# Kernel tuning notes

Hardware: AMD Instinct MI355X
Metric: run time of the kernel (lower is better)

## Reference

```python
import jax, jax.numpy as jnp
import numpy as np

K = 10      # neighbors; conv width math 10 -> 3 -> 1
EPS = 1e-5  # InstanceNorm2d default eps (affine=False)
NEG = 0.2   # leaky relu slope


def _instnorm(x):
    m = x.mean(axis=(2, 3), keepdims=True)
    v = x.var(axis=(2, 3), keepdims=True)  # biased var, as in torch instance_norm
    return (x - m) * jax.lax.rsqrt(v + EPS)


def _conv13(x, w, b, s):
    y = jax.lax.conv_general_dilated(x, w, (1, s), 'VALID',
                                     dimension_numbers=('NCHW', 'OIHW', 'NCHW'))
    return y + b[None, :, None, None]


def _block(x, wA, bA, wB, bB):
    # Sequential(conv(1,3,stride(1,3)), IN, ReLU, conv(1,3), IN, ReLU)
    y = jax.nn.relu(_instnorm(_conv13(x, wA, bA, 3)))
    return jax.nn.relu(_instnorm(_conv13(y, wB, bB, 1)))


def _knn_idx(coords, k):
    # coords [B,2,N] -> k nearest neighbor indices [B,N,k] (self excluded)
    pts = coords.transpose(0, 2, 1)
    sq = (pts ** 2).sum(-1)
    dist = sq[:, :, None] + sq[:, None, :] - 2.0 * jnp.einsum('bnc,bmc->bnm', pts, pts)
    dist = jnp.clip(dist, 1e-12)
    _, idx = jax.lax.top_k(-dist, k + 1)  # smallest distances, sorted
    return idx[:, :, 1:]


def _gather_nb(x, idx):
    # x [B,C,N], idx [B,N,k] -> [B,C,N,k]
    return jax.vmap(lambda f, i: f[:, i])(x, idx)


def _graph_feat(feats, idx):
    nb = _gather_nb(feats, idx)
    ctr = jnp.broadcast_to(feats[..., None], nb.shape)
    return jnp.concatenate([ctr, nb - ctr], axis=1)  # [B,2C,N,k]


def _cos_angle(coords, idx):
    nei = _gather_nb(coords, idx)          # [B,2,N,k]
    ctr = coords[..., None]                # [B,2,N,1]
    dot = (ctr * nei).sum(axis=1, keepdims=True)
    na = jnp.sqrt((ctr ** 2).sum(axis=1, keepdims=True))
    nb = jnp.sqrt((nei ** 2).sum(axis=1, keepdims=True))
    return dot / (na * nb)                 # [B,1,N,k]


def _c1(w, x):
    # 1x1 conv, no bias
    return jnp.einsum('oi,bihw->bohw', w, x)


def _forward(coords, features, W1, W2, W3, W3o, a1wA, a1bA, a1wB, a1bB,
             a2wA, a2bA, a2wB, a2bB, angwA, angbA, angwB, angbB):
    B, C, N = features.shape
    lrelu = lambda x: jax.nn.leaky_relu(x, NEG)
    x0 = features[..., None]
    # KNN depends only on coords: all three torch graph builds give identical indices
    idx = _knn_idx(coords, K)
    x1_old = _graph_feat(features, idx)                         # [B,2C,N,K]
    x1 = _block(x1_old, a1wA, a1bA, a1wB, a1bB)                 # [B,C,N,1]
    # angle_enc1 is shared and idx identical -> f_ang1 == f_ang2
    f_ang = _block(_cos_angle(coords, idx), angwA, angbA, angwB, angbB)
    x2 = _block(_graph_feat(x1[..., 0], idx), a2wA, a2bA, a2wB, a2bB)
    x3 = jnp.concatenate([x0, x1 + f_ang, x2 + f_ang], axis=1)  # [B,3C,N,1]
    x3 = lrelu(_instnorm(_c1(W3, x3))).reshape(B, -1, N)
    x1o = lrelu(_instnorm(_c1(W1, x1_old))).max(axis=-1, keepdims=True)   # [B,C,N,1]
    x2o = lrelu(_instnorm(_c1(W2, _graph_feat(x1o[..., 0], idx)))).max(axis=-1, keepdims=True)
    x3o = jnp.concatenate([x0, x1o, x2o], axis=1)               # [B,4C,N,1]
    x3o = lrelu(_instnorm(_c1(W3o, x3o))).reshape(B, -1, N)
    return x3 + x3o


def setup_inputs():
    key = jax.random.key(0)
    ks = jax.random.split(key, 20)
    B, C, N = 4, 128, 4096
    r = lambda i, shp, sc=1.0: jax.random.normal(ks[i], shp, jnp.float32) * sc
    s = 0.05
    return {
        'coords': r(0, (B, 2, N)),
        'features': r(1, (B, C, N)),
        'W1': r(2, (C, 2 * C), s),
        'W2': r(3, (2 * C, 2 * C), s),
        'W3': r(4, (C, 3 * C), s),
        'W3o': r(5, (C, 4 * C), s),
        'a1wA': r(6, (C, 2 * C, 1, 3), s), 'a1bA': r(7, (C,), s),
        'a1wB': r(8, (C, C, 1, 3), s), 'a1bB': r(9, (C,), s),
        'a2wA': r(10, (C, 2 * C, 1, 3), s), 'a2bA': r(11, (C,), s),
        'a2wB': r(12, (C, C, 1, 3), s), 'a2bB': r(13, (C,), s),
        'angwA': r(14, (C, 1, 1, 3), s), 'angbA': r(15, (C,), s),
        'angwB': r(16, (C, C, 1, 3), s), 'angbB': r(17, (C,), s),
    }


def reference(coords, features, W1, W2, W3, W3o, a1wA, a1bA, a1wB, a1bB,
              a2wA, a2bA, a2wB, a2bB, angwA, angbA, angwB, angbB):
    return _forward(coords, features, W1, W2, W3, W3o, a1wA, a1bA, a1wB, a1bB,
                    a2wA, a2bA, a2wB, a2bB, angwA, angbA, angwB, angbB)
```

## Files before the change

kernel.cpp:

```cpp
#include <hip/hip_runtime.h>
#include <hip/hip_bf16.h>

typedef unsigned long long ull;

#define BN 4
#define CH 128
#define NP 4096
#define KNB 10
#define EPSI 1e-5f
#define GM_PTS 16
#define CA_PTS 16

#define FMA4(A, W, F) do { (A).x += (W).x*(F); (A).y += (W).y*(F); \
                           (A).z += (W).z*(F); (A).w += (W).w*(F); } while(0)

__device__ __forceinline__ ull shfl_xor_u64(ull v, int mask) {
    unsigned lo = (unsigned)(v & 0xFFFFFFFFu);
    unsigned hi = (unsigned)(v >> 32);
    lo = __shfl_xor(lo, mask);
    hi = __shfl_xor(hi, mask);
    return ((ull)hi << 32) | lo;
}

__device__ __forceinline__ int clampj(int j) { return ((unsigned)j < (unsigned)NP) ? j : 0; }

__device__ __forceinline__ unsigned short f2bf(float f) {
    unsigned u = __float_as_uint(f);
    unsigned r = u + 0x7FFFu + ((u >> 16) & 1u);
    return (unsigned short)(r >> 16);
}
__device__ __forceinline__ float bf2f(unsigned short h) {
    return __uint_as_float(((unsigned)h) << 16);
}
__device__ __forceinline__ float4 bfload4(const unsigned short* p) {
    ushort4 h = *(const ushort4*)p;
    float4 r; r.x = bf2f(h.x); r.y = bf2f(h.y); r.z = bf2f(h.z); r.w = bf2f(h.w);
    return r;
}

__device__ __forceinline__ void d_packA(const float* w, unsigned short* WT, int i) {
    int co = i % CH, ci = (i / CH) % CH, s = i / (CH * CH);
    float val;
    if (s == 0) {
        val = 0.f;
        for (int dk = 0; dk < 3; dk++)
            val += w[(co * 256 + ci) * 3 + dk] - w[(co * 256 + 128 + ci) * 3 + dk];
    } else {
        val = w[(co * 256 + 128 + ci) * 3 + (s - 1)];
    }
    WT[i] = f2bf(val);
}
__device__ __forceinline__ void d_packB(const float* w, float* WT, int i) {
    int co = i % CH, ci = (i / CH) % CH, dk = i / (CH * CH);
    WT[i] = w[(co * CH + ci) * 3 + dk];
}
__device__ __forceinline__ void d_packUV(const float* w, float* Wu, float* Wn, int Cout, int i) {
    int co = i % Cout, ci = i / Cout;
    float a = w[co * 256 + ci], bb = w[co * 256 + 128 + ci];
    Wu[i] = a - bb; Wn[i] = bb;
}
__device__ __forceinline__ void d_packP(const float* w, float* WT, int Cin, int Cout, int i) {
    int co = i % Cout, ci = i / Cout;
    WT[i] = w[co * Cin + ci];
}

__global__ void pack_all(const float* __restrict__ a1wA, const float* __restrict__ a2wA,
                         const float* __restrict__ a1wB, const float* __restrict__ a2wB,
                         const float* __restrict__ angwB, const float* __restrict__ W1,
                         const float* __restrict__ W2, const float* __restrict__ W3,
                         const float* __restrict__ W3o, const float* __restrict__ angwA,
                         float* __restrict__ WA1T, float* __restrict__ WA2T,
                         float* __restrict__ WB1T, float* __restrict__ WB2T,
                         float* __restrict__ WBAT,
                         float* __restrict__ W1U, float* __restrict__ W1N,
                         float* __restrict__ W2U, float* __restrict__ W2N,
                         float* __restrict__ W3T, float* __restrict__ W3OT,
                         float* __restrict__ WANGA) {
    int i = blockIdx.x * 256 + threadIdx.x;
    const int sA = 4 * CH * CH;
    const int sB = 3 * CH * CH;
    if (i < sA) { d_packA(a1wA, (unsigned short*)WA1T, i); return; } i -= sA;
    if (i < sA) { d_packA(a2wA, (unsigned short*)WA2T, i); return; } i -= sA;
    if (i < sB) { d_packB(a1wB, WB1T, i); return; } i -= sB;
    if (i < sB) { d_packB(a2wB, WB2T, i); return; } i -= sB;
    if (i < sB) { d_packB(angwB, WBAT, i); return; } i -= sB;
    if (i < CH * CH) { d_packUV(W1, W1U, W1N, CH, i); return; } i -= CH * CH;
    if (i < CH * 256) { d_packUV(W2, W2U, W2N, 256, i); return; } i -= CH * 256;
    if (i < 384 * CH) { d_packP(W3, W3T, 384, CH, i); return; } i -= 384 * CH;
    if (i < 512 * CH) { d_packP(W3o, W3OT, 512, CH, i); return; } i -= 512 * CH;
    if (i < 3 * CH) { d_packP(angwA, WANGA, 3, CH, i); return; }
}

__global__ void ftrans_kernel(const float* __restrict__ feats, float* __restrict__ F) {
    int i = blockIdx.x * 256 + threadIdx.x;
    if (i >= BN * CH * NP) return;
    int n = i % NP, c = (i / NP) % CH, b = i / (NP * CH);
    F[(b * NP + n) * CH + c] = feats[i];
}

__global__ void knn_kernel(const float* __restrict__ coords, int* __restrict__ IDX) {
    int gw = blockIdx.x * 4 + (threadIdx.x >> 6);
    int b = gw / NP;
    int n = gw % NP;
    int lane = threadIdx.x & 63;
    float xn = coords[(b * 2 + 0) * NP + n];
    float yn = coords[(b * 2 + 1) * NP + n];
    float sn = __fadd_rn(__fmul_rn(xn, xn), __fmul_rn(yn, yn));
    ull a[11];
    #pragma unroll
    for (int q = 0; q < 11; q++) a[q] = 0xFFFFFFFFFFFFFFFFULL;
    for (int m = lane; m < NP; m += 64) {
        float xm = coords[(b * 2 + 0) * NP + m];
        float ym = coords[(b * 2 + 1) * NP + m];
        float sm = __fadd_rn(__fmul_rn(xm, xm), __fmul_rn(ym, ym));
        float dot = __fmaf_rn(yn, ym, __fmul_rn(xn, xm));
        float d = __fsub_rn(__fadd_rn(sn, sm), __fmul_rn(2.0f, dot));
        d = fmaxf(d, 1e-12f);
        ull key = ((ull)__float_as_uint(d) << 32) | (unsigned)m;
        if (key < a[10]) {
            a[10] = key;
            #pragma unroll
            for (int q = 10; q > 0; --q)
                if (a[q] < a[q - 1]) { ull t = a[q]; a[q] = a[q - 1]; a[q - 1] = t; }
        }
    }
    for (int r = 0; r < 11; ++r) {
        ull k = a[0];
        ull mk = k;
        #pragma unroll
        for (int off = 1; off < 64; off <<= 1) {
            ull o = shfl_xor_u64(mk, off);
            mk = (o < mk) ? o : mk;
        }
        if (k == mk) {
            #pragma unroll
            for (int q = 0; q < 10; ++q) a[q] = a[q + 1];
            a[10] = 0xFFFFFFFFFFFFFFFFULL;
        }
        if (lane == 0 && r > 0) IDX[(b * NP + n) * KNB + (r - 1)] = (int)(mk & 0xFFFFFFFFu);
    }
}

__global__ void cosangle_kernel(const float* __restrict__ coords, const int* __restrict__ IDX,
                                float* __restrict__ COSA) {
    int i = blockIdx.x * 256 + threadIdx.x;
    if (i >= BN * NP * KNB) return;
    int n = (i / KNB) % NP, b = i / (KNB * NP);
    int j = clampj(IDX[i]);
    float xc = coords[(b * 2 + 0) * NP + n], yc = coords[(b * 2 + 1) * NP + n];
    float xm = coords[(b * 2 + 0) * NP + j], ym = coords[(b * 2 + 1) * NP + j];
    float dot = xc * xm + yc * ym;
    float na = sqrtf(xc * xc + yc * yc);
    float nb2 = sqrtf(xm * xm + ym * ym);
    COSA[i] = dot / fmaxf(na * nb2, 1e-30f);
}

__global__ __launch_bounds__(256) void convA_kernel(const float* __restrict__ Fin,
                             const int* __restrict__ IDX,
                             const float* __restrict__ WT, float* __restrict__ YA,
                             float* __restrict__ PART,
                             const float* __restrict__ STATS, int slot) {
    __shared__ __align__(16) float ctr[CA_PTS][CH];
    __shared__ __align__(16) unsigned short nbh[CA_PTS][9][CH];
    __shared__ int jidx[CA_PTS * 9];
    int b = blockIdx.x / (NP / CA_PTS);
    int chunk = blockIdx.x % (NP / CA_PTS);
    int n0 = chunk * CA_PTS;
    int cog = threadIdx.x & 31;
    int pg  = threadIdx.x >> 5;
    const float* SB = (slot >= 0) ? &STATS[((size_t)(slot * BN + b) * 256) * 2] : nullptr;
    if (threadIdx.x < CA_PTS * 9) {
        int n = threadIdx.x / 9, kk = threadIdx.x % 9;
        jidx[threadIdx.x] = clampj(IDX[(b * NP + n0 + n) * KNB + kk]);
    }
    __syncthreads();
    for (int v4 = threadIdx.x; v4 < CA_PTS * 32; v4 += 256) {
        int n = v4 >> 5, c4 = v4 & 31;
        float4 x = *(const float4*)&Fin[(size_t)(b * NP + n0 + n) * CH + c4 * 4];
        if (SB) {
            float4 s0 = *(const float4*)&SB[c4 * 8];
            float4 s1 = *(const float4*)&SB[c4 * 8 + 4];
            x.x = fmaxf((x.x - s0.x) * s0.y, 0.f);
            x.y = fmaxf((x.y - s0.z) * s0.w, 0.f);
            x.z = fmaxf((x.z - s1.x) * s1.y, 0.f);
            x.w = fmaxf((x.w - s1.z) * s1.w, 0.f);
        }
        *(float4*)&ctr[n][c4 * 4] = x;
    }
    for (int v4 = threadIdx.x; v4 < CA_PTS * 9 * 32; v4 += 256) {
        int n = v4 / 288, rem = v4 % 288, kk = rem >> 5, c4 = rem & 31;
        float4 x = *(const float4*)&Fin[(size_t)(b * NP + jidx[n * 9 + kk]) * CH + c4 * 4];
        if (SB) {
            float4 s0 = *(const float4*)&SB[c4 * 8];
            float4 s1 = *(const float4*)&SB[c4 * 8 + 4];
            x.x = fmaxf((x.x - s0.x) * s0.y, 0.f);
            x.y = fmaxf((x.y - s0.z) * s0.w, 0.f);
            x.z = fmaxf((x.z - s1.x) * s1.y, 0.f);
            x.w = fmaxf((x.w - s1.z) * s1.w, 0.f);
        }
        ushort4 h;
        h.x = f2bf(x.x); h.y = f2bf(x.y); h.z = f2bf(x.z); h.w = f2bf(x.w);
        *(ushort4*)&nbh[n][kk][c4 * 4] = h;
    }
    __syncthreads();
    const ushort4* W4 = (const ushort4*)WT;
    const int p0 = pg * 2, p1 = pg * 2 + 1;
    float4 cacc0, cacc1;
    cacc0.x = cacc0.y = cacc0.z = cacc0.w = 0.f;
    cacc1 = cacc0;
    for (int ci = 0; ci < CH; ci += 4) {
        float4 xa = *(const float4*)&ctr[p0][ci];
        float4 xb = *(const float4*)&ctr[p1][ci];
        #pragma unroll
        for (int u = 0; u < 4; ++u) {
            ushort4 hw = W4[(ci + u) * 32 + cog];
            float4 w; w.x = bf2f(hw.x); w.y = bf2f(hw.y); w.z = bf2f(hw.z); w.w = bf2f(hw.w);
            float fa = ((const float*)&xa)[u];
            float fb = ((const float*)&xb)[u];
            FMA4(cacc0, w, fa); FMA4(cacc1, w, fb);
        }
    }
    float4 t00 = cacc0, t01 = cacc0, t02 = cacc0;
    float4 t10 = cacc1, t11 = cacc1, t12 = cacc1;
    for (int dk = 0; dk < 3; ++dk) {
        const ushort4* Wd = W4 + (size_t)(1 + dk) * (CH * 32);
        const unsigned short* a00 = &nbh[p0][0 * 3 + dk][0];
        const unsigned short* a01 = &nbh[p0][1 * 3 + dk][0];
        const unsigned short* a02 = &nbh[p0][2 * 3 + dk][0];
        const unsigned short* a10 = &nbh[p1][0 * 3 + dk][0];
        const unsigned short* a11 = &nbh[p1][1 * 3 + dk][0];
        const unsigned short* a12 = &nbh[p1][2 * 3 + dk][0];
        for (int ci = 0; ci < CH; ci += 4) {
            float4 x00 = bfload4(&a00[ci]);
            float4 x01 = bfload4(&a01[ci]);
            float4 x02 = bfload4(&a02[ci]);
            float4 x10 = bfload4(&a10[ci]);
            float4 x11 = bfload4(&a11[ci]);
            float4 x12 = bfload4(&a12[ci]);
            #pragma unroll
            for (int u = 0; u < 4; ++u) {
                ushort4 hw = Wd[(ci + u) * 32 + cog];
                float4 w; w.x = bf2f(hw.x); w.y = bf2f(hw.y); w.z = bf2f(hw.z); w.w = bf2f(hw.w);
                FMA4(t00, w, ((const float*)&x00)[u]);
                FMA4(t01, w, ((const float*)&x01)[u]);
                FMA4(t02, w, ((const float*)&x02)[u]);
                FMA4(t10, w, ((const float*)&x10)[u]);
                FMA4(t11, w, ((const float*)&x11)[u]);
                FMA4(t12, w, ((const float*)&x12)[u]);
            }
        }
    }
    {
        size_t base0 = ((size_t)(b * NP + n0 + p0) * 3) * CH + cog * 4;
        *(float4*)&YA[base0 + 0 * CH] = t00;
        *(float4*)&YA[base0 + 1 * CH] = t01;
        *(float4*)&YA[base0 + 2 * CH] = t02;
        size_t base1 = ((size_t)(b * NP + n0 + p1) * 3) * CH + cog * 4;
        *(float4*)&YA[base1 + 0 * CH] = t10;
        *(float4*)&YA[base1 + 1 * CH] = t11;
        *(float4*)&YA[base1 + 2 * CH] = t12;
    }
    float s4[4], q4[4];
    s4[0] = t00.x + t01.x + t02.x + t10.x + t11.x + t12.x;
    s4[1] = t00.y + t01.y + t02.y + t10.y + t11.y + t12.y;
    s4[2] = t00.z + t01.z + t02.z + t10.z + t11.z + t12.z;
    s4[3] = t00.w + t01.w + t02.w + t10.w + t11.w + t12.w;
    q4[0] = t00.x*t00.x + t01.x*t01.x + t02.x*t02.x + t10.x*t10.x + t11.x*t11.x + t12.x*t12.x;
    q4[1] = t00.y*t00.y + t01.y*t01.y + t02.y*t02.y + t10.y*t10.y + t11.y*t11.y + t12.y*t12.y;
    q4[2] = t00.z*t00.z + t01.z*t01.z + t02.z*t02.z + t10.z*t10.z + t11.z*t11.z + t12.z*t12.z;
    q4[3] = t00.w*t00.w + t01.w*t01.w + t02.w*t02.w + t10.w*t10.w + t11.w*t11.w + t12.w*t12.w;
    __syncthreads();
    float* red = (float*)&nbh[0][0][0];
    #pragma unroll
    for (int j = 0; j < 4; ++j) {
        red[((pg * 32 + cog) * 4 + j) * 2 + 0] = s4[j];
        red[((pg * 32 + cog) * 4 + j) * 2 + 1] = q4[j];
    }
    __syncthreads();
    if (threadIdx.x < CH) {
        int c = threadIdx.x;
        float ss = 0.f, qq = 0.f;
        #pragma unroll
        for (int g = 0; g < 8; ++g) {
            ss += red[((g * 32 + (c >> 2)) * 4 + (c & 3)) * 2 + 0];
            qq += red[((g * 32 + (c >> 2)) * 4 + (c & 3)) * 2 + 1];
        }
        PART[((size_t)(b * (NP / CA_PTS) + chunk) * 256 + c) * 2 + 0] = ss;
        PART[((size_t)(b * (NP / CA_PTS) + chunk) * 256 + c) * 2 + 1] = qq;
    }
}

__global__ void angA_kernel(const float* __restrict__ COSA, const float* __restrict__ WT,
                            float* __restrict__ YA, float* __restrict__ PART) {
    __shared__ float ca[32][10];
    int b = blockIdx.x / (NP / 32);
    int chunk = blockIdx.x % (NP / 32);
    int n0 = chunk * 32;
    int co = threadIdx.x;
    for (int v = threadIdx.x; v < 320; v += 128) {
        int nn = v / 10, kk = v % 10;
        ca[nn][kk] = COSA[(b * NP + n0 + nn) * KNB + kk];
    }
    float w0 = WT[co], w1 = WT[CH + co], w2 = WT[2 * CH + co];
    __syncthreads();
    float sum = 0.f, sq = 0.f;
    for (int nn = 0; nn < 32; nn++) {
        #pragma unroll
        for (int t = 0; t < 3; t++) {
            float v = w0 * ca[nn][3 * t] + w1 * ca[nn][3 * t + 1] + w2 * ca[nn][3 * t + 2];
            YA[((b * NP + n0 + nn) * 3 + t) * CH + co] = v;
            sum += v; sq += v * v;
        }
    }
    PART[((b * (NP / 32) + chunk) * 256 + co) * 2 + 0] = sum;
    PART[((b * (NP / 32) + chunk) * 256 + co) * 2 + 1] = sq;
}

template <int CIN, int NCOG>
__device__ __forceinline__ void gemm_16pt(const float* lds, const float* __restrict__ WT,
                                          int cog, int pg, float4 acc[4]) {
    const float4* W4 = (const float4*)WT;
    const float* xb = lds + pg * 4 * CIN;
    for (int ci = 0; ci < CIN; ci += 4) {
        float4 x0 = *(const float4*)&xb[0 * CIN + ci];
        float4 x1 = *(const float4*)&xb[1 * CIN + ci];
        float4 x2 = *(const float4*)&xb[2 * CIN + ci];
        float4 x3 = *(const float4*)&xb[3 * CIN + ci];
        #pragma unroll
        for (int u = 0; u < 4; ++u) {
            float4 w = W4[(ci + u) * NCOG + cog];
            float f0 = ((const float*)&x0)[u];
            float f1 = ((const float*)&x1)[u];
            float f2 = ((const float*)&x2)[u];
            float f3 = ((const float*)&x3)[u];
            FMA4(acc[0], w, f0); FMA4(acc[1], w, f1);
            FMA4(acc[2], w, f2); FMA4(acc[3], w, f3);
        }
    }
}

template <int NCOG>
__device__ __forceinline__ void reduce_stats(const float* s4, const float* q4,
                                             float* red, float* __restrict__ PART,
                                             int b, int chunk, int nchunks,
                                             int pg, int cog) {
    constexpr int COUT = NCOG * 4;
    __syncthreads();
    #pragma unroll
    for (int j = 0; j < 4; ++j) {
        red[((pg * NCOG + cog) * 4 + j) * 2 + 0] = s4[j];
        red[((pg * NCOG + cog) * 4 + j) * 2 + 1] = q4[j];
    }
    __syncthreads();
    int c = threadIdx.x;
    if (c < COUT) {
        float ss = 0.f, qq = 0.f;
        #pragma unroll
        for (int g = 0; g < 4; ++g) {
            ss += red[((g * NCOG + (c >> 2)) * 4 + (c & 3)) * 2 + 0];
            qq += red[((g * NCOG + (c >> 2)) * 4 + (c & 3)) * 2 + 1];
        }
        PART[((size_t)(b * nchunks + chunk) * 256 + c) * 2 + 0] = ss;
        PART[((size_t)(b * nchunks + chunk) * 256 + c) * 2 + 1] = qq;
    }
}

template <int NCOG>
__device__ __forceinline__ void out16(const float4 acc[4], float* __restrict__ OUT,
                                      int b, int n0, int pg, int cog,
                                      float s4[4], float q4[4]) {
    constexpr int COUT = NCOG * 4;
    #pragma unroll
    for (int p = 0; p < 4; ++p) {
        *(float4*)&OUT[(size_t)(b * NP + n0 + pg * 4 + p) * COUT + cog * 4] = acc[p];
        s4[0] += acc[p].x; s4[1] += acc[p].y; s4[2] += acc[p].z; s4[3] += acc[p].w;
        q4[0] += acc[p].x * acc[p].x; q4[1] += acc[p].y * acc[p].y;
        q4[2] += acc[p].z * acc[p].z; q4[3] += acc[p].w * acc[p].w;
    }
}

template <int CIN, int NCOG>
__global__ void pixel_gemm_t(const float* __restrict__ IN_, const float* __restrict__ WT,
                             float* __restrict__ OUT, const float* __restrict__ STATS,
                             int slot, int act, float* __restrict__ PART) {
    constexpr int COUT = NCOG * 4;
    constexpr int BD = 4 * NCOG;
    __shared__ __align__(16) float ldsin[16 * CIN];
    int b = blockIdx.x / (NP / 16);
    int chunk = blockIdx.x % (NP / 16);
    int n0 = chunk * 16;
    int cog = threadIdx.x & (NCOG - 1);
    int pg = threadIdx.x / NCOG;
    constexpr int nv4 = 16 * CIN / 4;
    if (slot >= 0) {
        int cbase = (4 * threadIdx.x) & 127;
        const float* st = &STATS[((slot * BN + b) * 256 + cbase) * 2];
        float m0 = st[0], r0 = st[1], m1 = st[2], r1 = st[3];
        float m2 = st[4], r2 = st[5], m3 = st[6], r3 = st[7];
        for (int v4 = threadIdx.x; v4 < nv4; v4 += BD) {
            float4 x = *(const float4*)&IN_[(size_t)(b * NP + n0) * CIN + 4 * v4];
            float v0 = (x.x - m0) * r0, v1 = (x.y - m1) * r1;
            float v2 = (x.z - m2) * r2, v3 = (x.w - m3) * r3;
            if (act) {
                x.x = (v0 >= 0.f) ? v0 : 0.2f * v0;
                x.y = (v1 >= 0.f) ? v1 : 0.2f * v1;
                x.z = (v2 >= 0.f) ? v2 : 0.2f * v2;
                x.w = (v3 >= 0.f) ? v3 : 0.2f * v3;
            } else {
                x.x = fmaxf(v0, 0.f); x.y = fmaxf(v1, 0.f);
                x.z = fmaxf(v2, 0.f); x.w = fmaxf(v3, 0.f);
            }
            *(float4*)&ldsin[4 * v4] = x;
        }
    } else {
        for (int v4 = threadIdx.x; v4 < nv4; v4 += BD)
            *(float4*)&ldsin[4 * v4] =
                *(const float4*)&IN_[(size_t)(b * NP + n0) * CIN + 4 * v4];
    }
    __syncthreads();
    float4 acc[4];
    #pragma unroll
    for (int p = 0; p < 4; ++p) acc[p].x = acc[p].y = acc[p].z = acc[p].w = 0.f;
    gemm_16pt<CIN, NCOG>(ldsin, WT, cog, pg, acc);
    float s4[4] = {0,0,0,0}, q4[4] = {0,0,0,0};
    out16<NCOG>(acc, OUT, b, n0, pg, cog, s4, q4);
    if (PART)
        reduce_stats<NCOG>(s4, q4, ldsin, PART, b, chunk, NP / 16, pg, cog);
}

__global__ void stats_final(const float* __restrict__ PART, float* __restrict__ STATS,
                            int S, int Cc, int slot, int nch) {
    __shared__ float ssum[256], ssq[256];
    int bc = blockIdx.x;
    int b = bc / Cc, c = bc % Cc;
    float sum = 0.f, sq = 0.f;
    for (int ch = threadIdx.x; ch < nch; ch += 256) {
        sum += PART[((b * nch + ch) * 256 + c) * 2 + 0];
        sq  += PART[((b * nch + ch) * 256 + c) * 2 + 1];
    }
    ssum[threadIdx.x] = sum; ssq[threadIdx.x] = sq;
    __syncthreads();
    for (int s = 128; s > 0; s >>= 1) {
        if (threadIdx.x < s) {
            ssum[threadIdx.x] += ssum[threadIdx.x + s];
            ssq[threadIdx.x]  += ssq[threadIdx.x + s];
        }
        __syncthreads();
    }
    if (threadIdx.x == 0) {
        float mean = ssum[0] / (float)S;
        float var = fmaxf(ssq[0] / (float)S - mean * mean, 0.f);
        STATS[((slot * BN + b) * 256 + c) * 2 + 0] = mean;
        STATS[((slot * BN + b) * 256 + c) * 2 + 1] = rsqrtf(var + EPSI);
    }
}

template <int NCOG>
__global__ void gathermax_t(const float* __restrict__ X, const float* __restrict__ Wu,
                            const float* __restrict__ V, const int* __restrict__ IDX,
                            float* __restrict__ M, float* __restrict__ PART,
                            const float* __restrict__ STATS, int slot) {
    constexpr int COUT = NCOG * 4;
    __shared__ __align__(16) float rows[GM_PTS * CH];
    int b = blockIdx.x / (NP / GM_PTS);
    int chunk = blockIdx.x % (NP / GM_PTS);
    int n0 = chunk * GM_PTS;
    int cog = threadIdx.x & (NCOG - 1);
    int pg = threadIdx.x / NCOG;
    if (slot >= 0) {
        int c0 = (4 * threadIdx.x) & 127;
        const float* st = &STATS[((slot * BN + b) * 256 + c0) * 2];
        float m0 = st[0], r0 = st[1], m1 = st[2], r1 = st[3];
        float m2 = st[4], r2 = st[5], m3 = st[6], r3 = st[7];
        for (int v4 = threadIdx.x; v4 < GM_PTS * CH / 4; v4 += COUT) {
            float4 x = *(const float4*)&X[(size_t)(b * NP + n0) * CH + v4 * 4];
            float v0 = (x.x - m0) * r0, v1 = (x.y - m1) * r1;
            float v2 = (x.z - m2) * r2, v3 = (x.w - m3) * r3;
            x.x = (v0 >= 0.f) ? v0 : 0.2f * v0;
            x.y = (v1 >= 0.f) ? v1 : 0.2f * v1;
            x.z = (v2 >= 0.f) ? v2 : 0.2f * v2;
            x.w = (v3 >= 0.f) ? v3 : 0.2f * v3;
            *(float4*)&rows[v4 * 4] = x;
        }
    } else {
        for (int v4 = threadIdx.x; v4 < GM_PTS * CH / 4; v4 += COUT)
            *(float4*)&rows[v4 * 4] = *(const float4*)&X[(size_t)(b * NP + n0) * CH + v4 * 4];
    }
    __syncthreads();
    float4 acc[4];
    #pragma unroll
    for (int p = 0; p < 4; ++p) acc[p].x = acc[p].y = acc[p].z = acc[p].w = 0.f;
    gemm_16pt<CH, NCOG>(rows, Wu, cog, pg, acc);
    float s4[4] = {0,0,0,0}, q4[4] = {0,0,0,0};
    #pragma unroll
    for (int p = 0; p < 4; ++p) {
        int nn = n0 + pg * 4 + p;
        float4 u = acc[p];
        float4 best; best.x = best.y = best.z = best.w = -3.4e38f;
        for (int k = 0; k < KNB; ++k) {
            int j = clampj(IDX[(b * NP + nn) * KNB + k]);
            float4 vv = *(const float4*)&V[(size_t)(b * NP + j) * COUT + cog * 4];
            vv.x += u.x; vv.y += u.y; vv.z += u.z; vv.w += u.w;
            s4[0] += vv.x; s4[1] += vv.y; s4[2] += vv.z; s4[3] += vv.w;
            q4[0] += vv.x * vv.x; q4[1] += vv.y * vv.y;
            q4[2] += vv.z * vv.z; q4[3] += vv.w * vv.w;
            best.x = fmaxf(best.x, vv.x); best.y = fmaxf(best.y, vv.y);
            best.z = fmaxf(best.z, vv.z); best.w = fmaxf(best.w, vv.w);
        }
        *(float4*)&M[(size_t)(b * NP + nn) * COUT + cog * 4] = best;
    }
    __syncthreads();
    reduce_stats<NCOG>(s4, q4, rows, PART, b, chunk, NP / GM_PTS, pg, cog);
}

__global__ void head3_kernel(const float* __restrict__ F, const float* __restrict__ X1,
                             const float* __restrict__ X2, const float* __restrict__ FANG,
                             const float* __restrict__ WT, float* __restrict__ Y3,
                             float* __restrict__ PART, const float* __restrict__ STATS) {
    __shared__ __align__(16) float lds[16 * 384];
    int b = blockIdx.x / (NP / 16);
    int chunk = blockIdx.x % (NP / 16);
    int n0 = chunk * 16;
    int cog = threadIdx.x & 31;
    int pg = threadIdx.x >> 5;
    const float* S1 = &STATS[((size_t)(1 * BN + b) * 256) * 2];
    const float* S5 = &STATS[((size_t)(5 * BN + b) * 256) * 2];
    const float* S3 = &STATS[((size_t)(3 * BN + b) * 256) * 2];
    for (int v4 = threadIdx.x; v4 < 16 * 96; v4 += 128) {
        int nn = v4 / 96, q4 = v4 % 96;
        int part = q4 >> 5, c4 = q4 & 31;
        size_t base = (size_t)(b * NP + n0 + nn) * CH + c4 * 4;
        float4 val;
        if (part == 0) val = *(const float4*)&F[base];
        else {
            const float* src = (part == 1) ? X1 : X2;
            const float* SX = (part == 1) ? S1 : S5;
            float4 xx = *(const float4*)&src[base];
            float4 aa = *(const float4*)&FANG[base];
            float4 sx0 = *(const float4*)&SX[c4 * 8];
            float4 sx1 = *(const float4*)&SX[c4 * 8 + 4];
            float4 sa0 = *(const float4*)&S3[c4 * 8];
            float4 sa1 = *(const float4*)&S3[c4 * 8 + 4];
            val.x = fmaxf((xx.x - sx0.x) * sx0.y, 0.f) + fmaxf((aa.x - sa0.x) * sa0.y, 0.f);
            val.y = fmaxf((xx.y - sx0.z) * sx0.w, 0.f) + fmaxf((aa.y - sa0.z) * sa0.w, 0.f);
            val.z = fmaxf((xx.z - sx1.x) * sx1.y, 0.f) + fmaxf((aa.z - sa1.x) * sa1.y, 0.f);
            val.w = fmaxf((xx.w - sx1.z) * sx1.w, 0.f) + fmaxf((aa.w - sa1.z) * sa1.w, 0.f);
        }
        *(float4*)&lds[v4 * 4] = val;
    }
    __syncthreads();
    float4 acc[4];
    #pragma unroll
    for (int p = 0; p < 4; ++p) acc[p].x = acc[p].y = acc[p].z = acc[p].w = 0.f;
    gemm_16pt<384, 32>(lds, WT, cog, pg, acc);
    float s4[4] = {0,0,0,0}, q4[4] = {0,0,0,0};
    out16<32>(acc, Y3, b, n0, pg, cog, s4, q4);
    reduce_stats<32>(s4, q4, lds, PART, b, chunk, NP / 16, pg, cog);
}

__global__ void head3o_kernel(const float* __restrict__ F, const float* __restrict__ X1O,
                              const float* __restrict__ X2O, const float* __restrict__ WT,
                              float* __restrict__ Y3O, float* __restrict__ PART,
                              const float* __restrict__ STATS) {
    __shared__ __align__(16) float lds[16 * 512];
    int b = blockIdx.x / (NP / 16);
    int chunk = blockIdx.x % (NP / 16);
    int n0 = chunk * 16;
    int cog = threadIdx.x & 31;
    int pg = threadIdx.x >> 5;
    const float* S6 = &STATS[((size_t)(6 * BN + b) * 256) * 2];
    const float* S7 = &STATS[((size_t)(7 * BN + b) * 256) * 2];
    for (int v4 = threadIdx.x; v4 < 16 * 128; v4 += 128) {
        int nn = v4 >> 7, q4 = v4 & 127;
        float4 val;
        if (q4 < 32) {
            val = *(const float4*)&F[(size_t)(b * NP + n0 + nn) * CH + q4 * 4];
        } else if (q4 < 64) {
            int c4 = q4 - 32;
            float4 x = *(const float4*)&X1O[(size_t)(b * NP + n0 + nn) * CH + c4 * 4];
            float4 s0 = *(const float4*)&S6[c4 * 8];
            float4 s1 = *(const float4*)&S6[c4 * 8 + 4];
            float v0 = (x.x - s0.x) * s0.y, v1 = (x.y - s0.z) * s0.w;
            float v2 = (x.z - s1.x) * s1.y, v3 = (x.w - s1.z) * s1.w;
            val.x = (v0 >= 0.f) ? v0 : 0.2f * v0;
            val.y = (v1 >= 0.f) ? v1 : 0.2f * v1;
            val.z = (v2 >= 0.f) ? v2 : 0.2f * v2;
            val.w = (v3 >= 0.f) ? v3 : 0.2f * v3;
        } else {
            int c4 = q4 - 64;
            float4 x = *(const float4*)&X2O[(size_t)(b * NP + n0 + nn) * 256 + c4 * 4];
            float4 s0 = *(const float4*)&S7[c4 * 8];
            float4 s1 = *(const float4*)&S7[c4 * 8 + 4];
            float v0 = (x.x - s0.x) * s0.y, v1 = (x.y - s0.z) * s0.w;
            float v2 = (x.z - s1.x) * s1.y, v3 = (x.w - s1.z) * s1.w;
            val.x = (v0 >= 0.f) ? v0 : 0.2f * v0;
            val.y = (v1 >= 0.f) ? v1 : 0.2f * v1;
            val.z = (v2 >= 0.f) ? v2 : 0.2f * v2;
            val.w = (v3 >= 0.f) ? v3 : 0.2f * v3;
        }
        *(float4*)&lds[v4 * 4] = val;
    }
    __syncthreads();
    float4 acc[4];
    #pragma unroll
    for (int p = 0; p < 4; ++p) acc[p].x = acc[p].y = acc[p].z = acc[p].w = 0.f;
    gemm_16pt<512, 32>(lds, WT, cog, pg, acc);
    float s4[4] = {0,0,0,0}, q4[4] = {0,0,0,0};
    out16<32>(acc, Y3O, b, n0, pg, cog, s4, q4);
    reduce_stats<32>(s4, q4, lds, PART, b, chunk, NP / 16, pg, cog);
}

__global__ void final_kernel(const float* __restrict__ Y3, const float* __restrict__ Y3O,
                             const float* __restrict__ STATS, float* __restrict__ out) {
    __shared__ float T[64][129];
    int b = blockIdx.x / (NP / 64);
    int n0 = (blockIdx.x % (NP / 64)) * 64;
    int co = threadIdx.x;
    float m3 = STATS[((8 * BN + b) * 256 + co) * 2 + 0];
    float r3 = STATS[((8 * BN + b) * 256 + co) * 2 + 1];
    float m3o = STATS[((9 * BN + b) * 256 + co) * 2 + 0];
    float r3o = STATS[((9 * BN + b) * 256 + co) * 2 + 1];
    for (int j = 0; j < 64; j++) {
        size_t idx = (size_t)(b * NP + n0 + j) * CH + co;
        float v3 = (Y3[idx] - m3) * r3;
        v3 = (v3 >= 0.f) ? v3 : 0.2f * v3;
        float v3o = (Y3O[idx] - m3o) * r3o;
        v3o = (v3o >= 0.f) ? v3o : 0.2f * v3o;
        T[j][co] = v3 + v3o;
    }
    __syncthreads();
    for (int rr = 0; rr < 64; rr++) {
        int r = rr * 2 + (threadIdx.x >> 6);
        int j = threadIdx.x & 63;
        out[(size_t)(b * CH + r) * NP + n0 + j] = T[j][r];
    }
}

extern "C" void kernel_launch(void* const* d_in, const int* in_sizes, int n_in,
                              void* d_out, int out_size, void* d_ws, size_t ws_size,
                              hipStream_t stream) {
    const float* coords   = (const float*)d_in[0];
    const float* features = (const float*)d_in[1];
    const float* W1   = (const float*)d_in[2];
    const float* W2   = (const float*)d_in[3];
    const float* W3   = (const float*)d_in[4];
    const float* W3o  = (const float*)d_in[5];
    const float* a1wA = (const float*)d_in[6];
    const float* a1wB = (const float*)d_in[8];
    const float* a2wA = (const float*)d_in[10];
    const float* a2wB = (const float*)d_in[12];
    const float* angwA = (const float*)d_in[14];
    const float* angwB = (const float*)d_in[16];
    float* out = (float*)d_out;
    float* ws = (float*)d_ws;
    (void)ws_size; (void)in_sizes; (void)n_in; (void)out_size;

    size_t off = 0;
    float* WA1T  = ws + off; off += 4 * CH * CH;
    float* WA2T  = ws + off; off += 4 * CH * CH;
    float* WB1T  = ws + off; off += 3 * CH * CH;
    float* WB2T  = ws + off; off += 3 * CH * CH;
    float* WBAT  = ws + off; off += 3 * CH * CH;
    float* WANGA = ws + off; off += 512;
    float* W1U   = ws + off; off += CH * CH;
    float* W1N   = ws + off; off += CH * CH;
    float* W2U   = ws + off; off += CH * 256;
    float* W2N   = ws + off; off += CH * 256;
    float* W3T   = ws + off; off += 384 * CH;
    float* W3OT  = ws + off; off += 512 * CH;
    int*   IDX   = (int*)(ws + off); off += (size_t)BN * NP * KNB;
    float* COSA  = ws + off; off += (size_t)BN * NP * KNB;
    float* PART  = ws + off; off += (size_t)BN * 1024 * 256 * 2;
    float* STATS = ws + off; off += 10 * BN * 256 * 2;
    const size_t UNIT = (size_t)BN * NP * CH;
    float* POOL  = ws + off; off += 7 * UNIT;

    float* F    = POOL + 0 * UNIT;
    float* YA   = POOL + 1 * UNIT;
    float* X1   = POOL + 4 * UNIT;
    float* FANG = POOL + 5 * UNIT;
    float* X2   = POOL + 6 * UNIT;
    float* Y3   = POOL + 1 * UNIT;
    float* V1   = POOL + 2 * UNIT;
    float* M1   = POOL + 6 * UNIT;
    float* V2   = POOL + 4 * UNIT;
    float* M2   = POOL + 2 * UNIT;
    float* Y3O  = POOL + 4 * UNIT;

    pack_all<<<1730, 256, 0, stream>>>(a1wA, a2wA, a1wB, a2wB, angwB, W1, W2, W3, W3o, angwA,
                                       WA1T, WA2T, WB1T, WB2T, WBAT,
                                       W1U, W1N, W2U, W2N, W3T, W3OT, WANGA);

    ftrans_kernel<<<(BN * CH * NP + 255) / 256, 256, 0, stream>>>(features, F);
    knn_kernel<<<BN * NP / 4, 256, 0, stream>>>(coords, IDX);
    cosangle_kernel<<<(BN * NP * KNB + 255) / 256, 256, 0, stream>>>(coords, IDX, COSA);

    auto sfin = [&](int S, int Cc, int slot, int nch) {
        stats_final<<<BN * Cc, 256, 0, stream>>>(PART, STATS, S, Cc, slot, nch);
    };

    convA_kernel<<<BN * (NP / CA_PTS), 256, 0, stream>>>(F, IDX, WA1T, YA, PART, STATS, -1);
    sfin(3 * NP, CH, 0, NP / CA_PTS);
    pixel_gemm_t<384, 32><<<BN * (NP / 16), 128, 0, stream>>>(YA, WB1T, X1, STATS, 0, 0, PART);
    sfin(NP, CH, 1, NP / 16);

    angA_kernel<<<BN * (NP / 32), 128, 0, stream>>>(COSA, WANGA, YA, PART);
    sfin(3 * NP, CH, 2, NP / 32);
    pixel_gemm_t<384, 32><<<BN * (NP / 16), 128, 0, stream>>>(YA, WBAT, FANG, STATS, 2, 0, PART);
    sfin(NP, CH, 3, NP / 16);

    convA_kernel<<<BN * (NP / CA_PTS), 256, 0, stream>>>(X1, IDX, WA2T, YA, PART, STATS, 1);
    sfin(3 * NP, CH, 4, NP / CA_PTS);
    pixel_gemm_t<384, 32><<<BN * (NP / 16), 128, 0, stream>>>(YA, WB2T, X2, STATS, 4, 0, PART);
    sfin(NP, CH, 5, NP / 16);

    head3_kernel<<<BN * (NP / 16), 128, 0, stream>>>(F, X1, X2, FANG, W3T, Y3, PART, STATS);
    sfin(NP, CH, 8, NP / 16);

    pixel_gemm_t<128, 32><<<BN * (NP / 16), 128, 0, stream>>>(F, W1N, V1, STATS, -1, 0, nullptr);
    gathermax_t<32><<<BN * (NP / GM_PTS), 128, 0, stream>>>(F, W1U, V1, IDX, M1, PART, STATS, -1);
    sfin(NP * KNB, CH, 6, NP / GM_PTS);

    pixel_gemm_t<128, 64><<<BN * (NP / 16), 256, 0, stream>>>(M1, W2N, V2, STATS, 6, 1, nullptr);
    gathermax_t<64><<<BN * (NP / GM_PTS), 256, 0, stream>>>(M1, W2U, V2, IDX, M2, PART, STATS, 6);
    sfin(NP * KNB, 256, 7, NP / GM_PTS);

    head3o_kernel<<<BN * (NP / 16), 128, 0, stream>>>(F, M1, M2, W3OT, Y3O, PART, STATS);
    sfin(NP, CH, 9, NP / 16);
    final_kernel<<<BN * (NP / 64), 128, 0, stream>>>(Y3, Y3O, STATS, out);
}
```

Baseline: 853.8 us.

## Restructure KNN as per-thread chunked scan with LDS tiles plus merge kernel

Replaces the one-wavefront-per-query KNN, which needed a cross-lane shuffle reduction to merge 64 top-11 lists, with a thread-per-query scan. Each block stages one quarter of the candidate coordinates in shared memory and keeps a private top-11 list per query. A second kernel merges the four partial lists per point into the final indices. This cuts global loads and shuffle merges, but the insertion branch now diverges across lanes, and it adds a scratch write/read pass plus one extra launch. Scratch reuses the PART buffer.

```diff
diff --git a/kernel.cpp b/kernel.cpp
--- a/kernel.cpp
+++ b/kernel.cpp
@@ -10,17 +10,11 @@
 #define EPSI 1e-5f
 #define GM_PTS 16
 #define CA_PTS 16
+#define KNN_CHUNKS 4
+#define KNN_CS (NP / KNN_CHUNKS)
 
 #define FMA4(A, W, F) do { (A).x += (W).x*(F); (A).y += (W).y*(F); \
                            (A).z += (W).z*(F); (A).w += (W).w*(F); } while(0)
-
-__device__ __forceinline__ ull shfl_xor_u64(ull v, int mask) {
-    unsigned lo = (unsigned)(v & 0xFFFFFFFFu);
-    unsigned hi = (unsigned)(v >> 32);
-    lo = __shfl_xor(lo, mask);
-    hi = __shfl_xor(hi, mask);
-    return ((ull)hi << 32) | lo;
-}
 
 __device__ __forceinline__ int clampj(int j) { return ((unsigned)j < (unsigned)NP) ? j : 0; }
 
@@ -98,47 +92,75 @@
     F[(b * NP + n) * CH + c] = feats[i];
 }
 
-__global__ void knn_kernel(const float* __restrict__ coords, int* __restrict__ IDX) {
-    int gw = blockIdx.x * 4 + (threadIdx.x >> 6);
-    int b = gw / NP;
-    int n = gw % NP;
-    int lane = threadIdx.x & 63;
+__global__ __launch_bounds__(64) void knn_scan(const float* __restrict__ coords,
+                                               ull* __restrict__ SCR) {
+    __shared__ __align__(16) float xs[KNN_CS];
+    __shared__ __align__(16) float ys[KNN_CS];
+    int bid = blockIdx.x;
+    int ptile = bid & 63;
+    int chunk = (bid >> 6) & (KNN_CHUNKS - 1);
+    int b = bid >> 8;
+    int lane = threadIdx.x;
+    int n = ptile * 64 + lane;
+    int c0 = chunk * KNN_CS;
+    for (int v = lane; v < KNN_CS / 4; v += 64) {
+        *(float4*)&xs[v * 4] = *(const float4*)&coords[(b * 2 + 0) * NP + c0 + v * 4];
+        *(float4*)&ys[v * 4] = *(const float4*)&coords[(b * 2 + 1) * NP + c0 + v * 4];
+    }
+    __syncthreads();
     float xn = coords[(b * 2 + 0) * NP + n];
     float yn = coords[(b * 2 + 1) * NP + n];
     float sn = __fadd_rn(__fmul_rn(xn, xn), __fmul_rn(yn, yn));
     ull a[11];
     #pragma unroll
     for (int q = 0; q < 11; q++) a[q] = 0xFFFFFFFFFFFFFFFFULL;
-    for (int m = lane; m < NP; m += 64) {
-        float xm = coords[(b * 2 + 0) * NP + m];
-        float ym = coords[(b * 2 + 1) * NP + m];
-        float sm = __fadd_rn(__fmul_rn(xm, xm), __fmul_rn(ym, ym));
-        float dot = __fmaf_rn(yn, ym, __fmul_rn(xn, xm));
-        float d = __fsub_rn(__fadd_rn(sn, sm), __fmul_rn(2.0f, dot));
-        d = fmaxf(d, 1e-12f);
-        ull key = ((ull)__float_as_uint(d) << 32) | (unsigned)m;
-        if (key < a[10]) {
-            a[10] = key;
-            #pragma unroll
-            for (int q = 10; q > 0; --q)
-                if (a[q] < a[q - 1]) { ull t = a[q]; a[q] = a[q - 1]; a[q - 1] = t; }
-        }
-    }
-    for (int r = 0; r < 11; ++r) {
-        ull k = a[0];
-        ull mk = k;
+    for (int c4 = 0; c4 < KNN_CS; c4 += 4) {
+        float4 x4 = *(const float4*)&xs[c4];
+        float4 y4 = *(const float4*)&ys[c4];
         #pragma unroll
-        for (int off = 1; off < 64; off <<= 1) {
-            ull o = shfl_xor_u64(mk, off);
-            mk = (o < mk) ? o : mk;
-        }
-        if (k == mk) {
-            #pragma unroll
-            for (int q = 0; q < 10; ++q) a[q] = a[q + 1];
-            a[10] = 0xFFFFFFFFFFFFFFFFULL;
-        }
-        if (lane == 0 && r > 0) IDX[(b * NP + n) * KNB + (r - 1)] = (int)(mk & 0xFFFFFFFFu);
-    }
+        for (int u = 0; u < 4; ++u) {
+            float xm = ((const float*)&x4)[u];
+            float ym = ((const float*)&y4)[u];
+            float sm = __fadd_rn(__fmul_rn(xm, xm), __fmul_rn(ym, ym));
+            float dot = __fmaf_rn(yn, ym, __fmul_rn(xn, xm));
+            float d = __fsub_rn(__fadd_rn(sn, sm), __fmul_rn(2.0f, dot));
+            d = fmaxf(d, 1e-12f);
+            ull key = ((ull)__float_as_uint(d) << 32) | (unsigned)(c0 + c4 + u);
+            if (key < a[10]) {
+                a[10] = key;
+                #pragma unroll
+                for (int q = 10; q > 0; --q)
+                    if (a[q] < a[q - 1]) { ull t = a[q]; a[q] = a[q - 1]; a[q - 1] = t; }
+            }
+        }
+    }
+    ull* o = &SCR[((size_t)(b * NP + n) * KNN_CHUNKS + chunk) * 11];
+    #pragma unroll
+    for (int q = 0; q < 11; ++q) o[q] = a[q];
+}
+
+__global__ __launch_bounds__(64) void knn_merge(const ull* __restrict__ SCR,
+                                                int* __restrict__ IDX) {
+    int pt = blockIdx.x * 64 + threadIdx.x;
+    const ull* s = &SCR[(size_t)pt * KNN_CHUNKS * 11];
+    ull a[11];
+    #pragma unroll
+    for (int q = 0; q < 11; ++q) a[q] = s[q];
+    for (int ch = 1; ch < KNN_CHUNKS; ++ch) {
+        #pragma unroll
+        for (int q = 0; q < 11; ++q) {
+            ull key = s[ch * 11 + q];
+            if (key < a[10]) {
+                a[10] = key;
+                #pragma unroll
+                for (int r = 10; r > 0; --r)
+                    if (a[r] < a[r - 1]) { ull t = a[r]; a[r] = a[r - 1]; a[r - 1] = t; }
+            }
+        }
+    }
+    #pragma unroll
+    for (int r = 1; r < 11; ++r)
+        IDX[pt * KNB + (r - 1)] = (int)(a[r] & 0xFFFFFFFFu);
 }
 
 __global__ void cosangle_kernel(const float* __restrict__ coords, const int* __restrict__ IDX,
@@ -687,12 +709,15 @@
     float* M2   = POOL + 2 * UNIT;
     float* Y3O  = POOL + 4 * UNIT;
 
+    ull* KNNSCR = (ull*)PART;
+
     pack_all<<<1730, 256, 0, stream>>>(a1wA, a2wA, a1wB, a2wB, angwB, W1, W2, W3, W3o, angwA,
                                        WA1T, WA2T, WB1T, WB2T, WBAT,
                                        W1U, W1N, W2U, W2N, W3T, W3OT, WANGA);
 
     ftrans_kernel<<<(BN * CH * NP + 255) / 256, 256, 0, stream>>>(features, F);
-    knn_kernel<<<BN * NP / 4, 256, 0, stream>>>(coords, IDX);
+    knn_scan<<<BN * KNN_CHUNKS * (NP / 64), 64, 0, stream>>>(coords, KNNSCR);
+    knn_merge<<<BN * NP / 64, 64, 0, stream>>>(KNNSCR, IDX);
     cosangle_kernel<<<(BN * NP * KNB + 255) / 256, 256, 0, stream>>>(coords, IDX, COSA);
 
     auto sfin = [&](int S, int Cc, int slot, int nch) {
```

After: 1.092 ms. 27.9% more time.
